# Optimization experiments

Measured on AMD Instinct MI355X. Metric: run time of the kernel, lower is better.

The kernel has to match this reference:

```python
import jax, jax.numpy as jnp
import numpy as np

B, S = 4, 2048
D_MODEL, N_HEADS, D_KV = 1024, 16, 64
NUM_BUCKETS, MAX_DIST = 32, 128


def _relative_position_bucket(relative_position, num_buckets=NUM_BUCKETS, max_distance=MAX_DIST):
    # bidirectional (encoder) variant, faithful to FlaxT5Attention._relative_position_bucket
    num_buckets = num_buckets // 2
    relative_buckets = (relative_position > 0).astype(jnp.int32) * num_buckets
    rp = jnp.abs(relative_position)
    max_exact = num_buckets // 2
    is_small = rp < max_exact
    rp_large = max_exact + (
        jnp.log(rp.astype(jnp.float32) / max_exact)
        / np.log(max_distance / max_exact)
        * (num_buckets - max_exact)
    )
    rp_large = jnp.minimum(rp_large, num_buckets - 1)
    return relative_buckets + jnp.where(is_small, rp, rp_large.astype(jnp.int32))


def setup_inputs() -> dict:
    key = jax.random.key(0)
    ks = jax.random.split(key, 6)
    return {
        "hidden_states": jax.random.normal(ks[0], (B, S, D_MODEL), jnp.float32),
        "mask": jnp.zeros((B, S), jnp.float32),  # additive mask, 0 = attend
        "wq": jax.random.normal(ks[1], (D_MODEL, N_HEADS * D_KV), jnp.float32) * 0.02,
        "wk": jax.random.normal(ks[2], (D_MODEL, N_HEADS * D_KV), jnp.float32) * 0.02,
        "wv": jax.random.normal(ks[3], (D_MODEL, N_HEADS * D_KV), jnp.float32) * 0.02,
        "wo": jax.random.normal(ks[4], (N_HEADS * D_KV, D_MODEL), jnp.float32) * 0.02,
        "rel_bias": jax.random.normal(ks[5], (NUM_BUCKETS, N_HEADS), jnp.float32) * 0.02,
    }


def reference(hidden_states, mask, wq, wk, wv, wo, rel_bias):
    b, s, _ = hidden_states.shape
    # QKV projections, split heads -> [B, S, H, D]
    q = (hidden_states @ wq).reshape(b, s, N_HEADS, D_KV)
    k = (hidden_states @ wk).reshape(b, s, N_HEADS, D_KV)
    v = (hidden_states @ wv).reshape(b, s, N_HEADS, D_KV)

    # relative position bias -> [1, H, S, S]
    pos = jnp.arange(s, dtype=jnp.int32)
    relative_position = pos[None, :] - pos[:, None]  # memory - query
    buckets = _relative_position_bucket(relative_position)
    position_bias = rel_bias[buckets].transpose(2, 0, 1)[None]  # [1,H,S,S]
    # encoder path: additive mask expanded to [B,1,1,K]
    position_bias = position_bias + mask[:, None, None, :]

    # flax dot_product_attention_weights scales q by 1/sqrt(depth)
    scores = jnp.einsum("bqhd,bkhd->bhqk", q / jnp.sqrt(jnp.float32(D_KV)), k)
    attn_weights = jax.nn.softmax(scores + position_bias, axis=-1)

    attn_output = jnp.einsum("bhqk,bkhd->bqhd", attn_weights, v)
    attn_output = attn_output.reshape(b, s, N_HEADS * D_KV) @ wo
    return attn_output, position_bias
```

## Files before the change

kernel.cpp:

```cpp
#include <hip/hip_runtime.h>
#include <hip/hip_bf16.h>

typedef __attribute__((ext_vector_type(8))) short bf16x8;
typedef __attribute__((ext_vector_type(8))) unsigned short u16x8;
typedef __attribute__((ext_vector_type(4))) float f32x4;

#define B_   4
#define S_   2048
#define H_   16
#define DKV  64
#define DM   1024

static __device__ __forceinline__ f32x4 mfma16(bf16x8 a, bf16x8 b, f32x4 c){
  return __builtin_amdgcn_mfma_f32_16x16x32_bf16(a, b, c, 0, 0, 0);
}
static __device__ __forceinline__ void gload_lds16(const void* g, void* l){
  __builtin_amdgcn_global_load_lds((const __attribute__((address_space(1))) void*)g,
                                   (__attribute__((address_space(3))) void*)l, 16, 0, 0);
}
static __device__ __forceinline__ unsigned short f2b(float f){
  union { __hip_bfloat16 b; unsigned short u; } x;
  x.b = __float2bfloat16(f);
  return x.u;
}

__global__ void prep_kernel(const float* __restrict__ hs, unsigned short* __restrict__ h_bf,
                            const float* __restrict__ w0, const float* __restrict__ w1,
                            const float* __restrict__ w2, const float* __restrict__ w3,
                            unsigned short* o0, unsigned short* o1,
                            unsigned short* o2, unsigned short* o3,
                            const float* __restrict__ rel_bias, float* __restrict__ table_t){
  __shared__ float tile[32][33];
  int bid = blockIdx.x, tid = threadIdx.x;
  if (bid < 8192){
    int i = bid * 256 + tid;
    float4 v = reinterpret_cast<const float4*>(hs)[i];
    ushort4 r;
    r.x = f2b(v.x); r.y = f2b(v.y); r.z = f2b(v.z); r.w = f2b(v.w);
    reinterpret_cast<ushort4*>(h_bf)[i] = r;
  } else if (bid < 12288){
    int t = bid - 8192;
    int z = t >> 10, by = (t >> 5) & 31, bx = t & 31;
    const float* src = (z==0) ? w0 : (z==1) ? w1 : (z==2) ? w2 : w3;
    unsigned short* dst = (z==0) ? o0 : (z==1) ? o1 : (z==2) ? o2 : o3;
    int tx = tid & 31, ty = tid >> 5;
    #pragma unroll
    for (int i = 0; i < 32; i += 8)
      tile[ty + i][tx] = src[(size_t)(by * 32 + ty + i) * DM + bx * 32 + tx];
    __syncthreads();
    #pragma unroll
    for (int i = 0; i < 32; i += 8)
      dst[(size_t)(bx * 32 + ty + i) * DM + by * 32 + tx] = f2b(tile[tx][ty + i]);
  } else {
    int i = (bid - 12288) * 256 + tid;
    if (i < 16 * 4095){
      int h = i / 4095;
      int idx = i - h * 4095;
      int rel = idx - 2047;
      int bucket = (rel > 0) ? 16 : 0;
      int rp = (rel < 0) ? -rel : rel;
      int off = (rp < 8) ? rp
              : 8 + (rp>=12) + (rp>=16) + (rp>=23) + (rp>=32) + (rp>=46) + (rp>=64) + (rp>=91);
      table_t[i] = rel_bias[(bucket + off) * 16 + h];
    }
  }
}

__global__ void posbias_kernel(const float* __restrict__ relb, const float* __restrict__ mask,
                               float* __restrict__ out){
  __shared__ float rbh[32];
  int row = blockIdx.x;
  int q = row & (S_ - 1);
  int h = (row >> 11) & (H_ - 1);
  int b = row >> 15;
  int tid = threadIdx.x;
  if (tid < 32) rbh[tid] = relb[tid * 16 + h];
  __syncthreads();
  const float* mrow = mask + b * S_;
  float* orow = out + (size_t)row * S_;
  int k0 = tid * 8;
  #pragma unroll
  for (int c = 0; c < 2; ++c){
    float4 mv = *(const float4*)(mrow + k0 + c * 4);
    float4 v;
    #pragma unroll
    for (int j = 0; j < 4; ++j){
      int k = k0 + c * 4 + j;
      int rel = k - q;
      int bucket = (rel > 0) ? 16 : 0;
      int rp = (rel < 0) ? -rel : rel;
      int off = (rp < 8) ? rp
              : 8 + (rp>=12) + (rp>=16) + (rp>=23) + (rp>=32) + (rp>=46) + (rp>=64) + (rp>=91);
      (&v.x)[j] = rbh[bucket + off] + (&mv.x)[j];
    }
    *(float4*)(orow + k0 + c*4) = v;
  }
}

template<int MODE>
__global__ __launch_bounds__(256, 2) void gemm_bt_kernel(
    const unsigned short* __restrict__ A, const unsigned short* __restrict__ Bt,
    void* __restrict__ outp, int M, int N, int K, float scale)
{
  __shared__ __align__(16) unsigned short As[2][128 * 32];
  __shared__ __align__(16) unsigned short Bs[2][128 * 32];
  int tid = threadIdx.x; int lane = tid & 63; int w = tid >> 6;
  int wr = w >> 1, wc = w & 1;
  int n0 = blockIdx.x * 128, m0 = blockIdx.y * 128;
  const char* Ab = (const char*)A;
  const char* Bb = (const char*)Bt;
  size_t Kb = (size_t)K * 2;

  f32x4 acc[4][4];
  #pragma unroll
  for (int i = 0; i < 4; ++i)
    #pragma unroll
    for (int j = 0; j < 4; ++j) acc[i][j] = (f32x4){0.f, 0.f, 0.f, 0.f};

  auto stage = [&](int kt, int bsel){
    size_t k0b = (size_t)kt * 64;
    #pragma unroll
    for (int c = 0; c < 2; ++c){
      int o = c * 4096 + w * 1024 + lane * 16;
      int row = o >> 6;
      int wbl = (o & 63) ^ (((row >> 1) & 3) << 4);
      gload_lds16(Ab + (size_t)(m0 + row) * Kb + k0b + wbl, (char*)As[bsel] + c * 4096 + w * 1024);
      gload_lds16(Bb + (size_t)(n0 + row) * Kb + k0b + wbl, (char*)Bs[bsel] + c * 4096 + w * 1024);
    }
  };

  int nk = K >> 5;
  int buf = 0;
  stage(0, 0);
  for (int kt = 0; kt < nk; ++kt){
    __syncthreads();
    if (kt + 1 < nk) stage(kt + 1, buf ^ 1);
    bf16x8 af[4], bfr[4];
    #pragma unroll
    for (int f = 0; f < 4; ++f){
      int row = wr * 64 + f * 16 + (lane & 15);
      int byt = (row * 64 + ((lane >> 4) * 16)) ^ (((row >> 1) & 3) << 4);
      af[f] = *(const bf16x8*)((const char*)As[buf] + byt);
    }
    #pragma unroll
    for (int f = 0; f < 4; ++f){
      int row = wc * 64 + f * 16 + (lane & 15);
      int byt = (row * 64 + ((lane >> 4) * 16)) ^ (((row >> 1) & 3) << 4);
      bfr[f] = *(const bf16x8*)((const char*)Bs[buf] + byt);
    }
    #pragma unroll
    for (int i = 0; i < 4; ++i)
      #pragma unroll
      for (int j = 0; j < 4; ++j)
        acc[i][j] = mfma16(af[i], bfr[j], acc[i][j]);
    buf ^= 1;
  }

  #pragma unroll
  for (int i = 0; i < 4; ++i){
    #pragma unroll
    for (int j = 0; j < 4; ++j){
      #pragma unroll
      for (int r = 0; r < 4; ++r){
        int m = m0 + wr * 64 + i * 16 + ((lane >> 4) * 4) + r;
        int n = n0 + wc * 64 + j * 16 + (lane & 15);
        if (MODE == 0){
          ((float*)outp)[(size_t)m * N + n] = acc[i][j][r] * scale;
        } else {
          int sel = n >> 10, nn = n & 1023;
          float v = acc[i][j][r] * (sel == 0 ? 0.125f : 1.0f);
          int b = m >> 11, s = m & 2047, hh = nn >> 6, d = nn & 63;
          ((unsigned short*)outp)[(size_t)sel * 8388608 +
              (((size_t)(b * H_ + hh) * S_) + s) * DKV + d] = f2b(v);
        }
      }
    }
  }
}

__global__ __launch_bounds__(256, 2) void attn_mfma_kernel(
    const unsigned short* __restrict__ Qp, const unsigned short* __restrict__ Kp,
    const unsigned short* __restrict__ Vp, const float* __restrict__ table_t,
    const float* __restrict__ mask, unsigned short* __restrict__ outp)
{
  __shared__ __align__(16) unsigned short Ks[2][64][72];
  __shared__ __align__(16) unsigned short Vs[2][64][72];
  __shared__ __align__(16) unsigned short Ps[4][32][72];
  __shared__ float bias_s[2][191];
  __shared__ float mask_s[2][64];

  int bid = blockIdx.x;
  int qt = bid & 15; int h = (bid >> 4) & 15; int b = bid >> 8;
  int qb = qt * 128;
  const unsigned short* qptr = Qp + ((size_t)(b * H_ + h) * S_ + qb) * DKV;
  const unsigned short* kptr = Kp + (size_t)(b * H_ + h) * S_ * DKV;
  const unsigned short* vptr = Vp + (size_t)(b * H_ + h) * S_ * DKV;
  int tid = threadIdx.x; int lane = tid & 63; int w = tid >> 6;

  bf16x8 qf[2][2];
  #pragma unroll
  for (int qs = 0; qs < 2; ++qs){
    const unsigned short* qrow = qptr + (size_t)(w * 32 + qs * 16 + (lane & 15)) * DKV + 8 * (lane >> 4);
    qf[qs][0] = *(const bf16x8*)qrow;
    qf[qs][1] = *(const bf16x8*)(qrow + 32);
  }
  float l_r[2][4] = {{0.f,0.f,0.f,0.f},{0.f,0.f,0.f,0.f}};
  f32x4 o_acc[2][4];
  #pragma unroll
  for (int qs = 0; qs < 2; ++qs)
    #pragma unroll
    for (int d = 0; d < 4; ++d) o_acc[qs][d] = (f32x4){0.f, 0.f, 0.f, 0.f};

  int bias_base = h * 4095 + (2047 - qb - 127);

  int skey = tid & 63;
  int sd0  = (tid >> 6) * 16;

  u16x8 ka, kb2, va, vb2;
  float biasr = 0.f, maskr = 0.f;
  auto gload = [&](int k0){
    const unsigned short* krow = kptr + (size_t)(k0 + skey) * DKV + sd0;
    const unsigned short* vrow = vptr + (size_t)(k0 + skey) * DKV + sd0;
    ka  = *(const u16x8*)krow;
    kb2 = *(const u16x8*)(krow + 8);
    va  = *(const u16x8*)vrow;
    vb2 = *(const u16x8*)(vrow + 8);
    if (tid < 191) biasr = table_t[bias_base + k0 + tid];
    else if (tid >= 192) maskr = mask[b * S_ + k0 + (tid - 192)];
  };
  auto lwrite = [&](int bsel){
    *(u16x8*)&Ks[bsel][skey][sd0]     = ka;
    *(u16x8*)&Ks[bsel][skey][sd0 + 8] = kb2;
    #pragma unroll
    for (int j = 0; j < 8; ++j){
      Vs[bsel][sd0 + j][skey]     = va[j];
      Vs[bsel][sd0 + 8 + j][skey] = vb2[j];
    }
    if (tid < 191) bias_s[bsel][tid] = biasr;
    else if (tid >= 192) mask_s[bsel][tid - 192] = maskr;
  };

  gload(0);
  lwrite(0);
  int cur = 0;
  for (int k0 = 0; k0 < S_; k0 += 64){
    __syncthreads();
    if (k0 + 64 < S_) gload(k0 + 64);

    bf16x8 kf[4][2];
    #pragma unroll
    for (int kb = 0; kb < 4; ++kb)
      #pragma unroll
      for (int ks = 0; ks < 2; ++ks)
        kf[kb][ks] = *(const bf16x8*)&Ks[cur][kb * 16 + (lane & 15)][ks * 32 + (lane >> 4) * 8];

    float t[2][4][4];
    float rs[2][4] = {{0.f,0.f,0.f,0.f},{0.f,0.f,0.f,0.f}};
    #pragma unroll
    for (int qs = 0; qs < 2; ++qs){
      f32x4 sc[4];
      #pragma unroll
      for (int kb = 0; kb < 4; ++kb){
        sc[kb] = (f32x4){0.f, 0.f, 0.f, 0.f};
        #pragma unroll
        for (int ks = 0; ks < 2; ++ks)
          sc[kb] = mfma16(qf[qs][ks], kf[kb][ks], sc[kb]);
      }
      #pragma unroll
      for (int kb = 0; kb < 4; ++kb){
        int k_l = kb * 16 + (lane & 15);
        float mk = mask_s[cur][k_l];
        #pragma unroll
        for (int r = 0; r < 4; ++r){
          int q_l = w * 32 + qs * 16 + (lane >> 4) * 4 + r;
          float p = __expf(sc[kb][r] + bias_s[cur][k_l - q_l + 127] + mk);
          t[qs][kb][r] = p;
          rs[qs][r] += p;
        }
      }
    }
    #pragma unroll
    for (int qs = 0; qs < 2; ++qs)
      #pragma unroll
      for (int r = 0; r < 4; ++r){
        #pragma unroll
        for (int off = 1; off < 16; off <<= 1)
          rs[qs][r] += __shfl_xor(rs[qs][r], off, 64);
        l_r[qs][r] += rs[qs][r];
      }
    #pragma unroll
    for (int qs = 0; qs < 2; ++qs)
      #pragma unroll
      for (int kb = 0; kb < 4; ++kb)
        #pragma unroll
        for (int r = 0; r < 4; ++r)
          Ps[w][qs * 16 + (lane >> 4) * 4 + r][kb * 16 + (lane & 15)] = f2b(t[qs][kb][r]);

    bf16x8 vf[4][2];
    #pragma unroll
    for (int db = 0; db < 4; ++db)
      #pragma unroll
      for (int ks = 0; ks < 2; ++ks)
        vf[db][ks] = *(const bf16x8*)&Vs[cur][db * 16 + (lane & 15)][ks * 32 + (lane >> 4) * 8];
    #pragma unroll
    for (int qs = 0; qs < 2; ++qs){
      bf16x8 pa[2];
      #pragma unroll
      for (int ks = 0; ks < 2; ++ks)
        pa[ks] = *(const bf16x8*)&Ps[w][qs * 16 + (lane & 15)][ks * 32 + (lane >> 4) * 8];
      #pragma unroll
      for (int db = 0; db < 4; ++db)
        #pragma unroll
        for (int ks = 0; ks < 2; ++ks)
          o_acc[qs][db] = mfma16(pa[ks], vf[db][ks], o_acc[qs][db]);
    }

    if (k0 + 64 < S_) lwrite(cur ^ 1);
    cur ^= 1;
  }

  #pragma unroll
  for (int qs = 0; qs < 2; ++qs)
    #pragma unroll
    for (int r = 0; r < 4; ++r){
      float inv = 1.0f / l_r[qs][r];
      int qg = qb + w * 32 + qs * 16 + (lane >> 4) * 4 + r;
      size_t rowoff = ((size_t)b * S_ + qg) * DM + h * DKV;
      #pragma unroll
      for (int db = 0; db < 4; ++db)
        outp[rowoff + db * 16 + (lane & 15)] = f2b(o_acc[qs][db][r] * inv);
    }
}

extern "C" void kernel_launch(void* const* d_in, const int* in_sizes, int n_in,
                              void* d_out, int out_size, void* d_ws, size_t ws_size,
                              hipStream_t stream) {
  const float* hs   = (const float*)d_in[0];
  const float* msk  = (const float*)d_in[1];
  const float* wq   = (const float*)d_in[2];
  const float* wk   = (const float*)d_in[3];
  const float* wv   = (const float*)d_in[4];
  const float* wo   = (const float*)d_in[5];
  const float* relb = (const float*)d_in[6];

  float* out_attn = (float*)d_out;
  float* out_pb   = (float*)d_out + (size_t)B_ * S_ * DM;

  const size_t SCRATCH_NEED = 76021760;
  char* ws = (ws_size >= SCRATCH_NEED && d_ws) ? (char*)d_ws : (char*)out_pb;

  unsigned short* h_bf  = (unsigned short*)(ws + 0);
  unsigned short* wqkv_t= (unsigned short*)(ws + 16777216);
  unsigned short* wk_t  = (unsigned short*)(ws + 18874368);
  unsigned short* wv_t  = (unsigned short*)(ws + 20971520);
  unsigned short* wo_t  = (unsigned short*)(ws + 23068672);
  unsigned short* qkv_b = (unsigned short*)(ws + 25165824);
  unsigned short* k_b   = (unsigned short*)(ws + 41943040);
  unsigned short* v_b   = (unsigned short*)(ws + 58720256);
  float*          tabl  = (float*)(ws + 75497472);

  prep_kernel<<<12544, 256, 0, stream>>>(hs, h_bf, wq, wk, wv, wo,
                                         wqkv_t, wk_t, wv_t, wo_t, relb, tabl);

  gemm_bt_kernel<1><<<dim3(24, 64), 256, 0, stream>>>(h_bf, wqkv_t, qkv_b, 8192, 3072, 1024, 1.0f);

  attn_mfma_kernel<<<B_ * H_ * 16, 256, 0, stream>>>(qkv_b, k_b, v_b, tabl, msk, h_bf);

  gemm_bt_kernel<0><<<dim3(8, 64), 256, 0, stream>>>(h_bf, wo_t, out_attn, 8192, 1024, 1024, 1.0f);

  posbias_kernel<<<B_ * H_ * S_, 256, 0, stream>>>(relb, msk, out_pb);
}
```

Before: 479.3 us.

## Fuse position-bias output writes into attention kernel when workspace available

The attention kernel now also writes the [B,H,S,S] position-bias output. Each block emits its 128 query rows spread over the 32 key tiles, four rows per tile, reading the transposed bias table and a mask row held in registers. This removes the separate posbias kernel launch and lets the large (~268MB) fp32 store stream overlap with attention compute. The fallback path keeps the old kernel sequence when no workspace is provided. The cost is extra global-store traffic and register pressure inside the attention loop.

```diff
diff --git a/kernel.cpp b/kernel.cpp
--- a/kernel.cpp
+++ b/kernel.cpp
@@ -178,10 +178,12 @@
   }
 }
 
+template<int PB>
 __global__ __launch_bounds__(256, 2) void attn_mfma_kernel(
     const unsigned short* __restrict__ Qp, const unsigned short* __restrict__ Kp,
     const unsigned short* __restrict__ Vp, const float* __restrict__ table_t,
-    const float* __restrict__ mask, unsigned short* __restrict__ outp)
+    const float* __restrict__ mask, unsigned short* __restrict__ outp,
+    float* __restrict__ pb_out)
 {
   __shared__ __align__(16) unsigned short Ks[2][64][72];
   __shared__ __align__(16) unsigned short Vs[2][64][72];
@@ -212,6 +214,16 @@
     for (int d = 0; d < 4; ++d) o_acc[qs][d] = (f32x4){0.f, 0.f, 0.f, 0.f};
 
   int bias_base = h * 4095 + (2047 - qb - 127);
+
+  const float* trow_h = table_t + h * 4095;
+  float4 mk0, mk1;
+  float* pb_base = nullptr;
+  if (PB){
+    const float* mrow = mask + b * S_ + tid * 8;
+    mk0 = *(const float4*)mrow;
+    mk1 = *(const float4*)(mrow + 4);
+    pb_base = pb_out + ((size_t)((b * H_ + h) * S_) + qb) * S_ + tid * 8;
+  }
 
   int skey = tid & 63;
   int sd0  = (tid >> 6) * 16;
@@ -243,7 +255,8 @@
   gload(0);
   lwrite(0);
   int cur = 0;
-  for (int k0 = 0; k0 < S_; k0 += 64){
+  int tile = 0;
+  for (int k0 = 0; k0 < S_; k0 += 64, ++tile){
     __syncthreads();
     if (k0 + 64 < S_) gload(k0 + 64);
 
@@ -315,6 +328,22 @@
           o_acc[qs][db] = mfma16(pa[ks], vf[db][ks], o_acc[qs][db]);
     }
 
+    if (PB){
+      #pragma unroll
+      for (int rr = 0; rr < 4; ++rr){
+        int q = qb + tile * 4 + rr;
+        const float* trow = trow_h + (2047 - q) + tid * 8;
+        float4 v0, v1;
+        v0.x = trow[0] + mk0.x; v0.y = trow[1] + mk0.y;
+        v0.z = trow[2] + mk0.z; v0.w = trow[3] + mk0.w;
+        v1.x = trow[4] + mk1.x; v1.y = trow[5] + mk1.y;
+        v1.z = trow[6] + mk1.z; v1.w = trow[7] + mk1.w;
+        float* orow = pb_base + (size_t)(tile * 4 + rr) * S_;
+        *(float4*)orow = v0;
+        *(float4*)(orow + 4) = v1;
+      }
+    }
+
     if (k0 + 64 < S_) lwrite(cur ^ 1);
     cur ^= 1;
   }
@@ -347,7 +376,8 @@
   float* out_pb   = (float*)d_out + (size_t)B_ * S_ * DM;
 
   const size_t SCRATCH_NEED = 76021760;
-  char* ws = (ws_size >= SCRATCH_NEED && d_ws) ? (char*)d_ws : (char*)out_pb;
+  bool ws_ok = (ws_size >= SCRATCH_NEED && d_ws);
+  char* ws = ws_ok ? (char*)d_ws : (char*)out_pb;
 
   unsigned short* h_bf  = (unsigned short*)(ws + 0);
   unsigned short* wqkv_t= (unsigned short*)(ws + 16777216);
@@ -364,9 +394,12 @@
 
   gemm_bt_kernel<1><<<dim3(24, 64), 256, 0, stream>>>(h_bf, wqkv_t, qkv_b, 8192, 3072, 1024, 1.0f);
 
-  attn_mfma_kernel<<<B_ * H_ * 16, 256, 0, stream>>>(qkv_b, k_b, v_b, tabl, msk, h_bf);
-
-  gemm_bt_kernel<0><<<dim3(8, 64), 256, 0, stream>>>(h_bf, wo_t, out_attn, 8192, 1024, 1024, 1.0f);
-
-  posbias_kernel<<<B_ * H_ * S_, 256, 0, stream>>>(relb, msk, out_pb);
-}
+  if (ws_ok){
+    attn_mfma_kernel<1><<<B_ * H_ * 16, 256, 0, stream>>>(qkv_b, k_b, v_b, tabl, msk, h_bf, out_pb);
+    gemm_bt_kernel<0><<<dim3(8, 64), 256, 0, stream>>>(h_bf, wo_t, out_attn, 8192, 1024, 1024, 1.0f);
+  } else {
+    attn_mfma_kernel<0><<<B_ * H_ * 16, 256, 0, stream>>>(qkv_b, k_b, v_b, tabl, msk, h_bf, nullptr);
+    gemm_bt_kernel<0><<<dim3(8, 64), 256, 0, stream>>>(h_bf, wo_t, out_attn, 8192, 1024, 1024, 1.0f);
+    posbias_kernel<<<B_ * H_ * S_, 256, 0, stream>>>(relb, msk, out_pb);
+  }
+}
```

Result: slower. 491.5 us (+2.5%).
